# Performance work log

Hardware: AMD Instinct MI355X
Metric: run time of the kernel (lower is better)

The kernel has to match this reference:

```python
import jax, jax.numpy as jnp
import numpy as np

K = 512
D = 64

def setup_inputs() -> dict:
    key = jax.random.key(0)
    k1, k2 = jax.random.split(key)
    z_e_x = jax.random.normal(k1, (64, 64, 64, 64), dtype=jnp.float32)  # [B, H, W, D]
    # nn.Embedding(K, D).weight.data.uniform_(-1/K, 1/K)
    codebook = jax.random.uniform(k2, (K, D), dtype=jnp.float32,
                                  minval=-1.0 / K, maxval=1.0 / K)
    return {"z_e_x": z_e_x, "codebook": codebook}

def reference(z_e_x, codebook):
    # vq(): nearest-codeword indices under squared L2 distance.
    flat = z_e_x.reshape(-1, z_e_x.shape[-1])            # [N, D]
    # ||z - e||^2 = ||z||^2 - 2 z.e + ||e||^2  (single fused expression)
    dists = (jnp.sum(flat * flat, axis=-1, keepdims=True)
             - 2.0 * flat @ codebook.T
             + jnp.sum(codebook * codebook, axis=-1))     # [N, K]
    indices = jnp.argmin(dists, axis=-1)                  # [N]
    return indices.reshape(z_e_x.shape[:-1])              # [B, H, W]
```

## Files before the change

kernel.cpp:

```cpp
#include <hip/hip_runtime.h>


typedef __attribute__((ext_vector_type(8))) short bf16x8;
typedef __attribute__((ext_vector_type(4))) float f32x4;

constexpr int DCB = 64;
constexpr size_t WS_CB    = 0;
constexpr size_t WS_CNORM = 65536;

static __device__ inline unsigned short f2bf(float f) {
  unsigned u = __float_as_uint(f);
  return (unsigned short)((u + 0x7FFFu + ((u >> 16) & 1u)) >> 16);
}

#define SWZ(row, b) (((row) << 7) + ((b) ^ (((row) & 7) << 4)))

__global__ __launch_bounds__(256) void vq_prep_kernel(
    const float* __restrict__ cb, unsigned char* __restrict__ ws)
{
  const int k = blockIdx.x * 256 + threadIdx.x;
  const float4* e4 = reinterpret_cast<const float4*>(cb + (size_t)k * DCB);
  float4 e[16];
  #pragma unroll
  for (int j = 0; j < 16; ++j) e[j] = e4[j];
  float s0 = 0.f, s1 = 0.f, s2 = 0.f, s3 = 0.f;
  #pragma unroll
  for (int j = 0; j < 16; ++j) {
    s0 = fmaf(e[j].x, e[j].x, s0); s1 = fmaf(e[j].y, e[j].y, s1);
    s2 = fmaf(e[j].z, e[j].z, s2); s3 = fmaf(e[j].w, e[j].w, s3);
  }
  ((float*)(ws + WS_CNORM))[k] = (s0 + s1) + (s2 + s3);

  const int r = k & 255;
  unsigned char* img = ws + WS_CB + (size_t)(k >> 8) * 32768 + (size_t)r * 128;
  #pragma unroll
  for (int c16 = 0; c16 < 8; ++c16) {
    uint4 w;
    w.x = (unsigned)f2bf(e[2*c16].x)   | ((unsigned)f2bf(e[2*c16].y)   << 16);
    w.y = (unsigned)f2bf(e[2*c16].z)   | ((unsigned)f2bf(e[2*c16].w)   << 16);
    w.z = (unsigned)f2bf(e[2*c16+1].x) | ((unsigned)f2bf(e[2*c16+1].y) << 16);
    w.w = (unsigned)f2bf(e[2*c16+1].z) | ((unsigned)f2bf(e[2*c16+1].w) << 16);
    *reinterpret_cast<uint4*>(img + ((c16 ^ (r & 7)) << 4)) = w;
  }
}

static __device__ inline void refine_rk(
    int row0, int row_local, int k,
    const float* __restrict__ z, const float* __restrict__ cb,
    const float* ArowSp, const float* cnormSp, unsigned long long* bestSp)
{
  const float* zr = z + (size_t)(row0 + row_local) * DCB;
  const float* e  = cb + (size_t)k * DCB;
  float d0 = 0.f, d1 = 0.f, d2 = 0.f, d3 = 0.f;
  #pragma unroll
  for (int j = 0; j < DCB; j += 4) {
    d0 = fmaf(zr[j + 0], e[j + 0], d0);
    d1 = fmaf(zr[j + 1], e[j + 1], d1);
    d2 = fmaf(zr[j + 2], e[j + 2], d2);
    d3 = fmaf(zr[j + 3], e[j + 3], d3);
  }
  const float dot = (d0 + d1) + (d2 + d3);
  const float A  = ArowSp[row_local];
  const float Ck = cnormSp[k];
  float dist;
  {
    #pragma clang fp contract(off)
    dist = (A - 2.0f * dot) + Ck;
  }
  unsigned long long packed =
      ((unsigned long long)__float_as_uint(dist) << 32) | (unsigned)k;
  atomicMin(bestSp + row_local, packed);
}

static __device__ inline bf16x8 pack8(float4 a, float4 b) {
  bf16x8 r;
  r[0] = (short)f2bf(a.x); r[1] = (short)f2bf(a.y);
  r[2] = (short)f2bf(a.z); r[3] = (short)f2bf(a.w);
  r[4] = (short)f2bf(b.x); r[5] = (short)f2bf(b.y);
  r[6] = (short)f2bf(b.z); r[7] = (short)f2bf(b.w);
  return r;
}

__global__ __launch_bounds__(512, 4) void vq_main_kernel(
    const float* __restrict__ z, const float* __restrict__ cb,
    const unsigned char* __restrict__ ws, int* __restrict__ out, int N)
{
  __shared__ unsigned short cbBf[512 * DCB];
  __shared__ float cnormS[512];
  __shared__ float ArowS[256];
  __shared__ float SrowS[256];
  __shared__ unsigned long long bestS[256];
  __shared__ unsigned ovfCnt[8];
  __shared__ unsigned ovfQ[8][64];

  const int tid = threadIdx.x;
  const int lane = tid & 63, wv = tid >> 6;
  const int g = lane >> 4, lm = lane & 15;
  const int row0 = blockIdx.x * 256;

  {
    const unsigned char* src = ws + WS_CB;
    #pragma unroll
    for (int q = 0; q < 8; ++q) {
      const int slab = wv * 8 + q;
      const unsigned char* gp = src + slab * 1024 + lane * 16;
      char* lp = (char*)cbBf + slab * 1024;
      __builtin_amdgcn_global_load_lds(
          (const __attribute__((address_space(1))) unsigned int*)gp,
          (__attribute__((address_space(3))) unsigned int*)lp, 16, 0, 0);
    }
  }
  cnormS[tid] = ((const float*)(ws + WS_CNORM))[tid];
  if (tid < 256) bestS[tid] = ~0ull;
  if (tid < 8) ovfCnt[tid] = 0u;
  if (tid < 256) {
    const float4* q4 = reinterpret_cast<const float4*>(z + (size_t)(row0 + tid) * DCB);
    float4 q[16];
    #pragma unroll
    for (int j = 0; j < 16; ++j) q[j] = q4[j];
    float A;
    {
      #pragma clang fp contract(off)
      float r0 = q[0].x*q[0].x, r1 = q[0].y*q[0].y, r2 = q[0].z*q[0].z, r3 = q[0].w*q[0].w;
      float r4 = q[1].x*q[1].x, r5 = q[1].y*q[1].y, r6 = q[1].z*q[1].z, r7 = q[1].w*q[1].w;
      #pragma unroll
      for (int a = 1; a < 8; ++a) {
        r0 += q[2*a].x*q[2*a].x;     r1 += q[2*a].y*q[2*a].y;
        r2 += q[2*a].z*q[2*a].z;     r3 += q[2*a].w*q[2*a].w;
        r4 += q[2*a+1].x*q[2*a+1].x; r5 += q[2*a+1].y*q[2*a+1].y;
        r6 += q[2*a+1].z*q[2*a+1].z; r7 += q[2*a+1].w*q[2*a+1].w;
      }
      A = ((r0 + r1) + (r2 + r3)) + ((r4 + r5) + (r6 + r7));
    }
    ArowS[tid] = A;
    float s0 = 0.f, s1 = 0.f, s2 = 0.f, s3 = 0.f;
    #pragma unroll
    for (int j = 0; j < 16; ++j) {
      s0 += fabsf(q[j].x); s1 += fabsf(q[j].y);
      s2 += fabsf(q[j].z); s3 += fabsf(q[j].w);
    }
    SrowS[tid] = (s0 + s1) + (s2 + s3);
  }
  bf16x8 afr[2][2];
  #pragma unroll
  for (int rt = 0; rt < 2; ++rt) {
    const float* zrow = z + (size_t)(row0 + wv * 32 + rt * 16 + lm) * DCB;
    #pragma unroll
    for (int s = 0; s < 2; ++s) {
      const float4 u0 = *reinterpret_cast<const float4*>(zrow + 32 * s + 8 * g);
      const float4 u1 = *reinterpret_cast<const float4*>(zrow + 32 * s + 8 * g + 4);
      afr[rt][s] = pack8(u0, u1);
    }
  }
  __syncthreads();

  float dmax[2][4];
  #pragma unroll
  for (int rt = 0; rt < 2; ++rt)
    #pragma unroll
    for (int i = 0; i < 4; ++i) dmax[rt][i] = -__builtin_inff();

  #pragma unroll
  for (int ct = 0; ct < 32; ++ct) {
    const int rowc = ct * 16 + lm;
    const bf16x8 b0 = *reinterpret_cast<const bf16x8*>((const char*)cbBf + SWZ(rowc, 16 * g));
    const bf16x8 b1 = *reinterpret_cast<const bf16x8*>((const char*)cbBf + SWZ(rowc, 16 * g + 64));
    f32x4 a0 = (f32x4)0.0f, a1 = (f32x4)0.0f;
    a0 = __builtin_amdgcn_mfma_f32_16x16x32_bf16(afr[0][0], b0, a0, 0, 0, 0);
    a0 = __builtin_amdgcn_mfma_f32_16x16x32_bf16(afr[0][1], b1, a0, 0, 0, 0);
    a1 = __builtin_amdgcn_mfma_f32_16x16x32_bf16(afr[1][0], b0, a1, 0, 0, 0);
    a1 = __builtin_amdgcn_mfma_f32_16x16x32_bf16(afr[1][1], b1, a1, 0, 0, 0);
    #pragma unroll
    for (int i = 0; i < 4; ++i) {
      dmax[0][i] = fmaxf(dmax[0][i], a0[i]);
      dmax[1][i] = fmaxf(dmax[1][i], a1[i]);
    }
  }

  #pragma unroll
  for (int mask = 1; mask <= 8; mask <<= 1)
    #pragma unroll
    for (int rt = 0; rt < 2; ++rt)
      #pragma unroll
      for (int i = 0; i < 4; ++i)
        dmax[rt][i] = fmaxf(dmax[rt][i], __shfl_xor(dmax[rt][i], mask));

  float thr[2][4];
  #pragma unroll
  for (int rt = 0; rt < 2; ++rt) {
    const float4 Sv = *reinterpret_cast<const float4*>(&SrowS[wv * 32 + rt * 16 + g * 4]);
    const float s4[4] = {Sv.x, Sv.y, Sv.z, Sv.w};
    #pragma unroll
    for (int i = 0; i < 4; ++i)
      thr[rt][i] = fmaf(-2.0f, dmax[rt][i],
                        fmaf(s4[i], 3.0517578125e-5f, 3.44140625e-4f));
  }

  unsigned c0 = 0, c1 = 0, c2 = 0, c3 = 0;
  int n = 0;
  #pragma unroll
  for (int ct = 0; ct < 32; ++ct) {
    const int rowc = ct * 16 + lm;
    const bf16x8 b0 = *reinterpret_cast<const bf16x8*>((const char*)cbBf + SWZ(rowc, 16 * g));
    const bf16x8 b1 = *reinterpret_cast<const bf16x8*>((const char*)cbBf + SWZ(rowc, 16 * g + 64));
    f32x4 a0 = (f32x4)0.0f, a1 = (f32x4)0.0f;
    a0 = __builtin_amdgcn_mfma_f32_16x16x32_bf16(afr[0][0], b0, a0, 0, 0, 0);
    a0 = __builtin_amdgcn_mfma_f32_16x16x32_bf16(afr[0][1], b1, a0, 0, 0, 0);
    a1 = __builtin_amdgcn_mfma_f32_16x16x32_bf16(afr[1][0], b0, a1, 0, 0, 0);
    a1 = __builtin_amdgcn_mfma_f32_16x16x32_bf16(afr[1][1], b1, a1, 0, 0, 0);
    const float Cc = cnormS[rowc];
    #pragma unroll
    for (int rt = 0; rt < 2; ++rt) {
      float core[4];
      #pragma unroll
      for (int i = 0; i < 4; ++i)
        core[i] = fmaf(-2.0f, (rt == 0 ? a0[i] : a1[i]), Cc);
      const float h = fmaxf(fmaxf(thr[rt][0] - core[0], thr[rt][1] - core[1]),
                            fmaxf(thr[rt][2] - core[2], thr[rt][3] - core[3]));
      if (__any(h >= 0.f)) {
        #pragma unroll
        for (int i = 0; i < 4; ++i) {
          if (core[i] <= thr[rt][i]) {
            const unsigned e = (unsigned)(ct * 8 + rt * 4 + i);
            if (n == 0) c0 = e; else if (n == 1) c1 = e;
            else if (n == 2) c2 = e; else if (n == 3) c3 = e;
            else {
              const unsigned rec = e | ((unsigned)g << 8) | ((unsigned)lm << 12);
              const unsigned slot = atomicAdd(&ovfCnt[wv], 1u);
              if (slot < 64u) ovfQ[wv][slot] = rec;
              else refine_rk(row0, wv * 32 + rt * 16 + g * 4 + i, ct * 16 + lm,
                             z, cb, ArowS, cnormS, bestS);
            }
            ++n;
          }
        }
      }
    }
  }

  const int nr = n < 4 ? n : 4;
  for (int t = 0; t < nr; ++t) {
    const unsigned e = (t == 0) ? c0 : (t == 1) ? c1 : (t == 2) ? c2 : c3;
    const int ct = (int)(e >> 3), rt = (int)((e >> 2) & 1u), i = (int)(e & 3u);
    refine_rk(row0, wv * 32 + rt * 16 + g * 4 + i, ct * 16 + lm,
              z, cb, ArowS, cnormS, bestS);
  }

  {
    unsigned cnt = ovfCnt[wv];
    cnt = cnt < 64u ? cnt : 64u;
    for (unsigned idx = (unsigned)lane; idx < cnt; idx += 64u) {
      const unsigned rec = ovfQ[wv][idx];
      const unsigned e = rec & 255u;
      const int ct = (int)(e >> 3), rt = (int)((e >> 2) & 1u), i = (int)(e & 3u);
      const int g2 = (int)((rec >> 8) & 3u), lm2 = (int)((rec >> 12) & 15u);
      refine_rk(row0, wv * 32 + rt * 16 + g2 * 4 + i, ct * 16 + lm2,
                z, cb, ArowS, cnormS, bestS);
    }
  }

  if (lane < 32) {
    const int r = wv * 32 + lane;
    out[row0 + r] = (int)(bestS[r] & 0xFFFFFFFFull);
  }
}

extern "C" void kernel_launch(void* const* d_in, const int* in_sizes, int n_in,
                              void* d_out, int out_size, void* d_ws, size_t ws_size,
                              hipStream_t stream) {
  const float* z  = (const float*)d_in[0];
  const float* cb = (const float*)d_in[1];
  int* out = (int*)d_out;
  unsigned char* ws = (unsigned char*)d_ws;

  const int N = in_sizes[0] / DCB;

  vq_prep_kernel<<<2, 256, 0, stream>>>(cb, ws);
  vq_main_kernel<<<N / 256, 512, 0, stream>>>(z, cb, ws, out, N);
}
```

Baseline: 163.1 us.

## Process 512 rows per block and route all candidates through shared queue

Doubles rows per block from 256 to 512, so each wave handles four 16-row tiles and each codebook LDS fragment feeds twice as many MFMAs. This halves the number of blocks, and with it the per-block codebook load into LDS. Candidate handling drops the per-lane register list and the wave-level __any guard: every candidate is pushed into a larger per-wave LDS queue via atomicAdd, and refine_rk is made noinline with partial unrolling to limit register pressure. The costs are higher VGPR use, more LDS atomics, and fewer blocks (512) to spread over the CUs.

Result: no change. 166.2 us (+1.9%).

```diff
diff --git a/kernel.cpp b/kernel.cpp
--- a/kernel.cpp
+++ b/kernel.cpp
@@ -44,7 +44,7 @@
   }
 }
 
-static __device__ inline void refine_rk(
+static __device__ __attribute__((noinline)) void refine_rk(
     int row0, int row_local, int k,
     const float* __restrict__ z, const float* __restrict__ cb,
     const float* ArowSp, const float* cnormSp, unsigned long long* bestSp)
@@ -87,16 +87,16 @@
 {
   __shared__ unsigned short cbBf[512 * DCB];
   __shared__ float cnormS[512];
-  __shared__ float ArowS[256];
-  __shared__ float SrowS[256];
-  __shared__ unsigned long long bestS[256];
-  __shared__ unsigned ovfCnt[8];
-  __shared__ unsigned ovfQ[8][64];
+  __shared__ float ArowS[512];
+  __shared__ float SrowS[512];
+  __shared__ unsigned long long bestS[512];
+  __shared__ unsigned qCnt[8];
+  __shared__ unsigned qBuf[8][128];
 
   const int tid = threadIdx.x;
   const int lane = tid & 63, wv = tid >> 6;
   const int g = lane >> 4, lm = lane & 15;
-  const int row0 = blockIdx.x * 256;
+  const int row0 = blockIdx.x * 512;
 
   {
     const unsigned char* src = ws + WS_CB;
@@ -111,9 +111,9 @@
     }
   }
   cnormS[tid] = ((const float*)(ws + WS_CNORM))[tid];
-  if (tid < 256) bestS[tid] = ~0ull;
-  if (tid < 8) ovfCnt[tid] = 0u;
-  if (tid < 256) {
+  bestS[tid] = ~0ull;
+  if (lane == 0) qCnt[wv] = 0u;
+  {
     const float4* q4 = reinterpret_cast<const float4*>(z + (size_t)(row0 + tid) * DCB);
     float4 q[16];
     #pragma unroll
@@ -141,10 +141,10 @@
     }
     SrowS[tid] = (s0 + s1) + (s2 + s3);
   }
-  bf16x8 afr[2][2];
-  #pragma unroll
-  for (int rt = 0; rt < 2; ++rt) {
-    const float* zrow = z + (size_t)(row0 + wv * 32 + rt * 16 + lm) * DCB;
+  bf16x8 afr[4][2];
+  #pragma unroll
+  for (int rt = 0; rt < 4; ++rt) {
+    const float* zrow = z + (size_t)(row0 + wv * 64 + rt * 16 + lm) * DCB;
     #pragma unroll
     for (int s = 0; s < 2; ++s) {
       const float4 u0 = *reinterpret_cast<const float4*>(zrow + 32 * s + 8 * g);
@@ -154,41 +154,47 @@
   }
   __syncthreads();
 
-  float dmax[2][4];
-  #pragma unroll
-  for (int rt = 0; rt < 2; ++rt)
+  float dmax[4][4];
+  #pragma unroll
+  for (int rt = 0; rt < 4; ++rt)
     #pragma unroll
     for (int i = 0; i < 4; ++i) dmax[rt][i] = -__builtin_inff();
 
-  #pragma unroll
+  #pragma unroll 8
   for (int ct = 0; ct < 32; ++ct) {
     const int rowc = ct * 16 + lm;
     const bf16x8 b0 = *reinterpret_cast<const bf16x8*>((const char*)cbBf + SWZ(rowc, 16 * g));
     const bf16x8 b1 = *reinterpret_cast<const bf16x8*>((const char*)cbBf + SWZ(rowc, 16 * g + 64));
-    f32x4 a0 = (f32x4)0.0f, a1 = (f32x4)0.0f;
+    f32x4 a0 = (f32x4)0.0f, a1 = (f32x4)0.0f, a2 = (f32x4)0.0f, a3 = (f32x4)0.0f;
     a0 = __builtin_amdgcn_mfma_f32_16x16x32_bf16(afr[0][0], b0, a0, 0, 0, 0);
     a0 = __builtin_amdgcn_mfma_f32_16x16x32_bf16(afr[0][1], b1, a0, 0, 0, 0);
     a1 = __builtin_amdgcn_mfma_f32_16x16x32_bf16(afr[1][0], b0, a1, 0, 0, 0);
     a1 = __builtin_amdgcn_mfma_f32_16x16x32_bf16(afr[1][1], b1, a1, 0, 0, 0);
+    a2 = __builtin_amdgcn_mfma_f32_16x16x32_bf16(afr[2][0], b0, a2, 0, 0, 0);
+    a2 = __builtin_amdgcn_mfma_f32_16x16x32_bf16(afr[2][1], b1, a2, 0, 0, 0);
+    a3 = __builtin_amdgcn_mfma_f32_16x16x32_bf16(afr[3][0], b0, a3, 0, 0, 0);
+    a3 = __builtin_amdgcn_mfma_f32_16x16x32_bf16(afr[3][1], b1, a3, 0, 0, 0);
     #pragma unroll
     for (int i = 0; i < 4; ++i) {
       dmax[0][i] = fmaxf(dmax[0][i], a0[i]);
       dmax[1][i] = fmaxf(dmax[1][i], a1[i]);
+      dmax[2][i] = fmaxf(dmax[2][i], a2[i]);
+      dmax[3][i] = fmaxf(dmax[3][i], a3[i]);
     }
   }
 
   #pragma unroll
   for (int mask = 1; mask <= 8; mask <<= 1)
     #pragma unroll
-    for (int rt = 0; rt < 2; ++rt)
+    for (int rt = 0; rt < 4; ++rt)
       #pragma unroll
       for (int i = 0; i < 4; ++i)
         dmax[rt][i] = fmaxf(dmax[rt][i], __shfl_xor(dmax[rt][i], mask));
 
-  float thr[2][4];
-  #pragma unroll
-  for (int rt = 0; rt < 2; ++rt) {
-    const float4 Sv = *reinterpret_cast<const float4*>(&SrowS[wv * 32 + rt * 16 + g * 4]);
+  float thr[4][4];
+  #pragma unroll
+  for (int rt = 0; rt < 4; ++rt) {
+    const float4 Sv = *reinterpret_cast<const float4*>(&SrowS[wv * 64 + rt * 16 + g * 4]);
     const float s4[4] = {Sv.x, Sv.y, Sv.z, Sv.w};
     #pragma unroll
     for (int i = 0; i < 4; ++i)
@@ -196,73 +202,55 @@
                         fmaf(s4[i], 3.0517578125e-5f, 3.44140625e-4f));
   }
 
-  unsigned c0 = 0, c1 = 0, c2 = 0, c3 = 0;
-  int n = 0;
-  #pragma unroll
+  #pragma unroll 8
   for (int ct = 0; ct < 32; ++ct) {
     const int rowc = ct * 16 + lm;
     const bf16x8 b0 = *reinterpret_cast<const bf16x8*>((const char*)cbBf + SWZ(rowc, 16 * g));
     const bf16x8 b1 = *reinterpret_cast<const bf16x8*>((const char*)cbBf + SWZ(rowc, 16 * g + 64));
-    f32x4 a0 = (f32x4)0.0f, a1 = (f32x4)0.0f;
+    f32x4 a0 = (f32x4)0.0f, a1 = (f32x4)0.0f, a2 = (f32x4)0.0f, a3 = (f32x4)0.0f;
     a0 = __builtin_amdgcn_mfma_f32_16x16x32_bf16(afr[0][0], b0, a0, 0, 0, 0);
     a0 = __builtin_amdgcn_mfma_f32_16x16x32_bf16(afr[0][1], b1, a0, 0, 0, 0);
     a1 = __builtin_amdgcn_mfma_f32_16x16x32_bf16(afr[1][0], b0, a1, 0, 0, 0);
     a1 = __builtin_amdgcn_mfma_f32_16x16x32_bf16(afr[1][1], b1, a1, 0, 0, 0);
+    a2 = __builtin_amdgcn_mfma_f32_16x16x32_bf16(afr[2][0], b0, a2, 0, 0, 0);
+    a2 = __builtin_amdgcn_mfma_f32_16x16x32_bf16(afr[2][1], b1, a2, 0, 0, 0);
+    a3 = __builtin_amdgcn_mfma_f32_16x16x32_bf16(afr[3][0], b0, a3, 0, 0, 0);
+    a3 = __builtin_amdgcn_mfma_f32_16x16x32_bf16(afr[3][1], b1, a3, 0, 0, 0);
     const float Cc = cnormS[rowc];
     #pragma unroll
-    for (int rt = 0; rt < 2; ++rt) {
-      float core[4];
+    for (int rt = 0; rt < 4; ++rt) {
       #pragma unroll
-      for (int i = 0; i < 4; ++i)
-        core[i] = fmaf(-2.0f, (rt == 0 ? a0[i] : a1[i]), Cc);
-      const float h = fmaxf(fmaxf(thr[rt][0] - core[0], thr[rt][1] - core[1]),
-                            fmaxf(thr[rt][2] - core[2], thr[rt][3] - core[3]));
-      if (__any(h >= 0.f)) {
-        #pragma unroll
-        for (int i = 0; i < 4; ++i) {
-          if (core[i] <= thr[rt][i]) {
-            const unsigned e = (unsigned)(ct * 8 + rt * 4 + i);
-            if (n == 0) c0 = e; else if (n == 1) c1 = e;
-            else if (n == 2) c2 = e; else if (n == 3) c3 = e;
-            else {
-              const unsigned rec = e | ((unsigned)g << 8) | ((unsigned)lm << 12);
-              const unsigned slot = atomicAdd(&ovfCnt[wv], 1u);
-              if (slot < 64u) ovfQ[wv][slot] = rec;
-              else refine_rk(row0, wv * 32 + rt * 16 + g * 4 + i, ct * 16 + lm,
-                             z, cb, ArowS, cnormS, bestS);
-            }
-            ++n;
-          }
+      for (int i = 0; i < 4; ++i) {
+        const float av = (rt == 0) ? a0[i] : (rt == 1) ? a1[i]
+                       : (rt == 2) ? a2[i] : a3[i];
+        const float core = fmaf(-2.0f, av, Cc);
+        if (core <= thr[rt][i]) {
+          const unsigned rec = (unsigned)ct | ((unsigned)rt << 5) |
+                               ((unsigned)i << 7) | ((unsigned)g << 9) |
+                               ((unsigned)lm << 11);
+          const unsigned slot = atomicAdd(&qCnt[wv], 1u);
+          if (slot < 128u) qBuf[wv][slot] = rec;
+          else refine_rk(row0, wv * 64 + rt * 16 + g * 4 + i, ct * 16 + lm,
+                         z, cb, ArowS, cnormS, bestS);
         }
       }
     }
   }
 
-  const int nr = n < 4 ? n : 4;
-  for (int t = 0; t < nr; ++t) {
-    const unsigned e = (t == 0) ? c0 : (t == 1) ? c1 : (t == 2) ? c2 : c3;
-    const int ct = (int)(e >> 3), rt = (int)((e >> 2) & 1u), i = (int)(e & 3u);
-    refine_rk(row0, wv * 32 + rt * 16 + g * 4 + i, ct * 16 + lm,
-              z, cb, ArowS, cnormS, bestS);
-  }
-
-  {
-    unsigned cnt = ovfCnt[wv];
-    cnt = cnt < 64u ? cnt : 64u;
+  {
+    unsigned cnt = qCnt[wv];
+    cnt = cnt < 128u ? cnt : 128u;
     for (unsigned idx = (unsigned)lane; idx < cnt; idx += 64u) {
-      const unsigned rec = ovfQ[wv][idx];
-      const unsigned e = rec & 255u;
-      const int ct = (int)(e >> 3), rt = (int)((e >> 2) & 1u), i = (int)(e & 3u);
-      const int g2 = (int)((rec >> 8) & 3u), lm2 = (int)((rec >> 12) & 15u);
-      refine_rk(row0, wv * 32 + rt * 16 + g2 * 4 + i, ct * 16 + lm2,
+      const unsigned rec = qBuf[wv][idx];
+      const int ct2 = (int)(rec & 31u), rt2 = (int)((rec >> 5) & 3u);
+      const int i2 = (int)((rec >> 7) & 3u), g2 = (int)((rec >> 9) & 3u);
+      const int lm2 = (int)((rec >> 11) & 15u);
+      refine_rk(row0, wv * 64 + rt2 * 16 + g2 * 4 + i2, ct2 * 16 + lm2,
                 z, cb, ArowS, cnormS, bestS);
     }
   }
 
-  if (lane < 32) {
-    const int r = wv * 32 + lane;
-    out[row0 + r] = (int)(bestS[r] & 0xFFFFFFFFull);
-  }
+  out[row0 + tid] = (int)(bestS[tid] & 0xFFFFFFFFull);
 }
 
 extern "C" void kernel_launch(void* const* d_in, const int* in_sizes, int n_in,
@@ -276,5 +264,5 @@
   const int N = in_sizes[0] / DCB;
 
   vq_prep_kernel<<<2, 256, 0, stream>>>(cb, ws);
-  vq_main_kernel<<<N / 256, 512, 0, stream>>>(z, cb, ws, out, N);
-}
+  vq_main_kernel<<<N / 512, 512, 0, stream>>>(z, cb, ws, out, N);
+}
```

## Double block size to 1024 threads and simplify candidate queueing for refinement

Applied to the files above, without the earlier changes.

Each block now handles 512 rows with 1024 threads, so the 64KB bf16 codebook staged in LDS is amortized over twice as many rows. Row norms are split across thread pairs and combined with a shuffle. The per-lane register candidate list is replaced by a shared atomic queue used for every candidate, refine_rk is made noinline, and the MFMA loops are unrolled only 4x. Together these aim to cut register pressure and per-block setup cost, at the price of more LDS atomics, possible queue overflow into inline refinement, and a launch-bounds hint of 8 that may cap registers tightly.

Measured after the change: 294.8 us. 1.81x slower.

```diff
diff --git a/kernel.cpp b/kernel.cpp
--- a/kernel.cpp
+++ b/kernel.cpp
@@ -44,7 +44,7 @@
   }
 }
 
-static __device__ inline void refine_rk(
+static __device__ __attribute__((noinline)) void refine_rk(
     int row0, int row_local, int k,
     const float* __restrict__ z, const float* __restrict__ cb,
     const float* ArowSp, const float* cnormSp, unsigned long long* bestSp)
@@ -81,28 +81,28 @@
   return r;
 }
 
-__global__ __launch_bounds__(512, 4) void vq_main_kernel(
+__global__ __launch_bounds__(1024, 8) void vq_main_kernel(
     const float* __restrict__ z, const float* __restrict__ cb,
     const unsigned char* __restrict__ ws, int* __restrict__ out, int N)
 {
   __shared__ unsigned short cbBf[512 * DCB];
   __shared__ float cnormS[512];
-  __shared__ float ArowS[256];
-  __shared__ float SrowS[256];
-  __shared__ unsigned long long bestS[256];
-  __shared__ unsigned ovfCnt[8];
-  __shared__ unsigned ovfQ[8][64];
+  __shared__ float ArowS[512];
+  __shared__ float SrowS[512];
+  __shared__ unsigned long long bestS[512];
+  __shared__ unsigned qCnt[16];
+  __shared__ unsigned qBuf[16][64];
 
   const int tid = threadIdx.x;
   const int lane = tid & 63, wv = tid >> 6;
   const int g = lane >> 4, lm = lane & 15;
-  const int row0 = blockIdx.x * 256;
+  const int row0 = blockIdx.x * 512;
 
   {
     const unsigned char* src = ws + WS_CB;
     #pragma unroll
-    for (int q = 0; q < 8; ++q) {
-      const int slab = wv * 8 + q;
+    for (int q = 0; q < 4; ++q) {
+      const int slab = wv * 4 + q;
       const unsigned char* gp = src + slab * 1024 + lane * 16;
       char* lp = (char*)cbBf + slab * 1024;
       __builtin_amdgcn_global_load_lds(
@@ -110,36 +110,42 @@
           (__attribute__((address_space(3))) unsigned int*)lp, 16, 0, 0);
     }
   }
-  cnormS[tid] = ((const float*)(ws + WS_CNORM))[tid];
-  if (tid < 256) bestS[tid] = ~0ull;
-  if (tid < 8) ovfCnt[tid] = 0u;
-  if (tid < 256) {
-    const float4* q4 = reinterpret_cast<const float4*>(z + (size_t)(row0 + tid) * DCB);
-    float4 q[16];
-    #pragma unroll
-    for (int j = 0; j < 16; ++j) q[j] = q4[j];
-    float A;
+  if (tid < 512) {
+    cnormS[tid] = ((const float*)(ws + WS_CNORM))[tid];
+    bestS[tid] = ~0ull;
+  }
+  if (tid < 16) qCnt[tid] = 0u;
+  {
+    const int row_l = tid >> 1;
+    const int par = tid & 1;
+    const float4* q4 = reinterpret_cast<const float4*>(
+        z + (size_t)(row0 + row_l) * DCB) + par;
+    float r0, r1, r2, r3, s0, s1, s2, s3;
     {
       #pragma clang fp contract(off)
-      float r0 = q[0].x*q[0].x, r1 = q[0].y*q[0].y, r2 = q[0].z*q[0].z, r3 = q[0].w*q[0].w;
-      float r4 = q[1].x*q[1].x, r5 = q[1].y*q[1].y, r6 = q[1].z*q[1].z, r7 = q[1].w*q[1].w;
+      float4 v = q4[0];
+      r0 = v.x * v.x; r1 = v.y * v.y; r2 = v.z * v.z; r3 = v.w * v.w;
+      s0 = fabsf(v.x); s1 = fabsf(v.y); s2 = fabsf(v.z); s3 = fabsf(v.w);
       #pragma unroll
       for (int a = 1; a < 8; ++a) {
-        r0 += q[2*a].x*q[2*a].x;     r1 += q[2*a].y*q[2*a].y;
-        r2 += q[2*a].z*q[2*a].z;     r3 += q[2*a].w*q[2*a].w;
-        r4 += q[2*a+1].x*q[2*a+1].x; r5 += q[2*a+1].y*q[2*a+1].y;
-        r6 += q[2*a+1].z*q[2*a+1].z; r7 += q[2*a+1].w*q[2*a+1].w;
+        v = q4[2 * a];
+        r0 += v.x * v.x; r1 += v.y * v.y; r2 += v.z * v.z; r3 += v.w * v.w;
+        s0 += fabsf(v.x); s1 += fabsf(v.y); s2 += fabsf(v.z); s3 += fabsf(v.w);
       }
-      A = ((r0 + r1) + (r2 + r3)) + ((r4 + r5) + (r6 + r7));
-    }
-    ArowS[tid] = A;
-    float s0 = 0.f, s1 = 0.f, s2 = 0.f, s3 = 0.f;
-    #pragma unroll
-    for (int j = 0; j < 16; ++j) {
-      s0 += fabsf(q[j].x); s1 += fabsf(q[j].y);
-      s2 += fabsf(q[j].z); s3 += fabsf(q[j].w);
-    }
-    SrowS[tid] = (s0 + s1) + (s2 + s3);
+    }
+    float p, sp;
+    {
+      #pragma clang fp contract(off)
+      p  = (r0 + r1) + (r2 + r3);
+      sp = (s0 + s1) + (s2 + s3);
+    }
+    const float po  = __shfl_xor(p, 1);
+    const float spo = __shfl_xor(sp, 1);
+    if (par == 0) {
+      #pragma clang fp contract(off)
+      ArowS[row_l] = p + po;
+      SrowS[row_l] = sp + spo;
+    }
   }
   bf16x8 afr[2][2];
   #pragma unroll
@@ -160,7 +166,7 @@
     #pragma unroll
     for (int i = 0; i < 4; ++i) dmax[rt][i] = -__builtin_inff();
 
-  #pragma unroll
+  #pragma unroll 4
   for (int ct = 0; ct < 32; ++ct) {
     const int rowc = ct * 16 + lm;
     const bf16x8 b0 = *reinterpret_cast<const bf16x8*>((const char*)cbBf + SWZ(rowc, 16 * g));
@@ -196,9 +202,7 @@
                         fmaf(s4[i], 3.0517578125e-5f, 3.44140625e-4f));
   }
 
-  unsigned c0 = 0, c1 = 0, c2 = 0, c3 = 0;
-  int n = 0;
-  #pragma unroll
+  #pragma unroll 4
   for (int ct = 0; ct < 32; ++ct) {
     const int rowc = ct * 16 + lm;
     const bf16x8 b0 = *reinterpret_cast<const bf16x8*>((const char*)cbBf + SWZ(rowc, 16 * g));
@@ -211,50 +215,32 @@
     const float Cc = cnormS[rowc];
     #pragma unroll
     for (int rt = 0; rt < 2; ++rt) {
-      float core[4];
       #pragma unroll
-      for (int i = 0; i < 4; ++i)
-        core[i] = fmaf(-2.0f, (rt == 0 ? a0[i] : a1[i]), Cc);
-      const float h = fmaxf(fmaxf(thr[rt][0] - core[0], thr[rt][1] - core[1]),
-                            fmaxf(thr[rt][2] - core[2], thr[rt][3] - core[3]));
-      if (__any(h >= 0.f)) {
-        #pragma unroll
-        for (int i = 0; i < 4; ++i) {
-          if (core[i] <= thr[rt][i]) {
-            const unsigned e = (unsigned)(ct * 8 + rt * 4 + i);
-            if (n == 0) c0 = e; else if (n == 1) c1 = e;
-            else if (n == 2) c2 = e; else if (n == 3) c3 = e;
-            else {
-              const unsigned rec = e | ((unsigned)g << 8) | ((unsigned)lm << 12);
-              const unsigned slot = atomicAdd(&ovfCnt[wv], 1u);
-              if (slot < 64u) ovfQ[wv][slot] = rec;
-              else refine_rk(row0, wv * 32 + rt * 16 + g * 4 + i, ct * 16 + lm,
-                             z, cb, ArowS, cnormS, bestS);
-            }
-            ++n;
-          }
+      for (int i = 0; i < 4; ++i) {
+        const float av = (rt == 0) ? a0[i] : a1[i];
+        const float core = fmaf(-2.0f, av, Cc);
+        if (core <= thr[rt][i]) {
+          const unsigned rec = (unsigned)ct | ((unsigned)rt << 5) |
+                               ((unsigned)i << 6) | ((unsigned)g << 8) |
+                               ((unsigned)lm << 10);
+          const unsigned slot = atomicAdd(&qCnt[wv], 1u);
+          if (slot < 64u) qBuf[wv][slot] = rec;
+          else refine_rk(row0, wv * 32 + rt * 16 + g * 4 + i, ct * 16 + lm,
+                         z, cb, ArowS, cnormS, bestS);
         }
       }
     }
   }
 
-  const int nr = n < 4 ? n : 4;
-  for (int t = 0; t < nr; ++t) {
-    const unsigned e = (t == 0) ? c0 : (t == 1) ? c1 : (t == 2) ? c2 : c3;
-    const int ct = (int)(e >> 3), rt = (int)((e >> 2) & 1u), i = (int)(e & 3u);
-    refine_rk(row0, wv * 32 + rt * 16 + g * 4 + i, ct * 16 + lm,
-              z, cb, ArowS, cnormS, bestS);
-  }
-
-  {
-    unsigned cnt = ovfCnt[wv];
+  {
+    unsigned cnt = qCnt[wv];
     cnt = cnt < 64u ? cnt : 64u;
     for (unsigned idx = (unsigned)lane; idx < cnt; idx += 64u) {
-      const unsigned rec = ovfQ[wv][idx];
-      const unsigned e = rec & 255u;
-      const int ct = (int)(e >> 3), rt = (int)((e >> 2) & 1u), i = (int)(e & 3u);
-      const int g2 = (int)((rec >> 8) & 3u), lm2 = (int)((rec >> 12) & 15u);
-      refine_rk(row0, wv * 32 + rt * 16 + g2 * 4 + i, ct * 16 + lm2,
+      const unsigned rec = qBuf[wv][idx];
+      const int ct2 = (int)(rec & 31u), rt2 = (int)((rec >> 5) & 1u);
+      const int i2 = (int)((rec >> 6) & 3u), g2 = (int)((rec >> 8) & 3u);
+      const int lm2 = (int)((rec >> 10) & 15u);
+      refine_rk(row0, wv * 32 + rt2 * 16 + g2 * 4 + i2, ct2 * 16 + lm2,
                 z, cb, ArowS, cnormS, bestS);
     }
   }
@@ -276,5 +262,5 @@
   const int N = in_sizes[0] / DCB;
 
   vq_prep_kernel<<<2, 256, 0, stream>>>(cb, ws);
-  vq_main_kernel<<<N / 256, 512, 0, stream>>>(z, cb, ws, out, N);
-}
+  vq_main_kernel<<<N / 512, 1024, 0, stream>>>(z, cb, ws, out, N);
+}
```
